# Kernel optimization log

Hardware: AMD Instinct MI355X
Metric: run time of the kernel (lower is better)

## Reference

```python
import jax, jax.numpy as jnp
import numpy as np
from jax import lax


def conv2d(x, w, b, stride, pad):
    # x: NCHW, w: OIHW (PyTorch Conv2d layout)
    y = lax.conv_general_dilated(x, w, (stride, stride), ((pad, pad), (pad, pad)),
                                 dimension_numbers=('NCHW', 'OIHW', 'NCHW'))
    return y + b[None, :, None, None]


def conv_transpose2d(x, w, b, stride, pad):
    # PyTorch ConvTranspose2d weight layout: (in_ch, out_ch, kH, kW).
    # Equivalent to a conv with lhs dilation, flipped kernel, in/out swapped.
    k = w.shape[2]
    w2 = jnp.transpose(jnp.flip(w, (2, 3)), (1, 0, 2, 3))  # (out, in, k, k)
    p = k - 1 - pad
    y = lax.conv_general_dilated(x, w2, (1, 1), ((p, p), (p, p)),
                                 lhs_dilation=(stride, stride),
                                 dimension_numbers=('NCHW', 'OIHW', 'NCHW'))
    return y + b[None, :, None, None]


def setup_inputs() -> dict:
    key = jax.random.key(0)
    ks = jax.random.split(key, 8)
    K, D = 512, 64  # num_embeddings, embedding_dim
    x = jax.random.uniform(ks[0], (32, 3, 256, 256), jnp.float32)

    def he(k, shape, fan_in):
        return jax.random.normal(k, shape, jnp.float32) * np.float32(np.sqrt(2.0 / fan_in))

    w1 = he(ks[1], (64, 3, 4, 4), 3 * 16);   b1 = jnp.zeros((64,), jnp.float32)
    w2 = he(ks[2], (D, 64, 4, 4), 64 * 16);  b2 = jnp.zeros((D,), jnp.float32)
    # codebook init: uniform(-1/K, 1/K) as in the torch module
    codebook = jax.random.uniform(ks[3], (K, D), jnp.float32, -1.0 / K, 1.0 / K)
    dw1 = he(ks[4], (D, 64, 4, 4), D * 16);  db1 = jnp.zeros((64,), jnp.float32)
    dw2 = he(ks[5], (64, 3, 4, 4), 64 * 16); db2 = jnp.zeros((3,), jnp.float32)
    return dict(x=x, w1=w1, b1=b1, w2=w2, b2=b2, codebook=codebook,
                dw1=dw1, db1=db1, dw2=dw2, db2=db2)


def reference(x, w1, b1, w2, b2, codebook, dw1, db1, dw2, db2):
    # Encoder
    z_e = jax.nn.relu(conv2d(x, w1, b1, 2, 1))
    z_e = jax.nn.relu(conv2d(z_e, w2, b2, 2, 1))  # (N, D, H/4, W/4)
    D = z_e.shape[1]
    # Faithful to torch: .view(-1, C) on contiguous NCHW (NO channel permute)
    zf = z_e.reshape(-1, D)  # (N*Hq*Wq, D) given D == Hq here numerically; rows are contiguous slices
    # ||z - e||^2 = ||z||^2 + ||e||^2 - 2 z.e  -> (M, K) distance matrix
    d = (jnp.sum(zf * zf, axis=1, keepdims=True)
         + jnp.sum(codebook * codebook, axis=1)
         - 2.0 * (zf @ codebook.T))
    idx = jnp.argmin(d, axis=1)           # (M,) int
    z_q = codebook[idx].reshape(z_e.shape)  # gather + reshape back to z_e shape
    # Decoder
    h = jax.nn.relu(conv_transpose2d(z_q, dw1, db1, 2, 1))
    x_recon = jax.nn.sigmoid(conv_transpose2d(h, dw2, db2, 2, 1))
    return x_recon, z_q
```

## Files before the change

### kernel.cpp

```cpp
#include <hip/hip_runtime.h>
#include <math.h>


typedef __attribute__((ext_vector_type(8))) short short8;
typedef __attribute__((ext_vector_type(4))) short short4v;
typedef __attribute__((ext_vector_type(4))) float f32x4;

#define MFMA16(a, b, c) __builtin_amdgcn_mfma_f32_16x16x32_bf16((a), (b), (c), 0, 0, 0)

__device__ __forceinline__ short f2bf(float f) {
  union { float f; unsigned u; } x; x.f = f;
  unsigned r = (x.u + 0x7FFFu + ((x.u >> 16) & 1u)) >> 16;
  return (short)r;
}
__device__ __forceinline__ float bf2f(short s) {
  union { unsigned u; float f; } x;
  x.u = ((unsigned)(unsigned short)s) << 16;
  return x.f;
}

__global__ __launch_bounds__(256) void k_prep(const float* __restrict__ w2,
                                              const float* __restrict__ dw1,
                                              const float* __restrict__ dw2,
                                              const float* __restrict__ cb,
                                              short* __restrict__ A2,
                                              short* __restrict__ AD1,
                                              short* __restrict__ AD2,
                                              short* __restrict__ cbb,
                                              float* __restrict__ cnm) {
  int i = blockIdx.x * 256 + threadIdx.x;
  {
    int t = i >> 12, oc = (i >> 6) & 63, c = i & 63;
    A2[i] = f2bf(w2[(oc * 64 + c) * 16 + t]);
  }
  {
    int p = i >> 14, ab = (i >> 12) & 3, oc = (i >> 6) & 63, c = i & 63;
    int kh = 1 - (p >> 1) + 2 * (ab >> 1);
    int kw = 1 - (p & 1) + 2 * (ab & 1);
    AD1[i] = f2bf(dw1[(c * 64 + oc) * 16 + kh * 4 + kw]);
  }
  if (i < 16384) {
    int p = i >> 12, ab = (i >> 10) & 3, oc = (i >> 6) & 15, c = i & 63;
    int kh = 1 - (p >> 1) + 2 * (ab >> 1);
    int kw = 1 - (p & 1) + 2 * (ab & 1);
    short v = 0;
    if (oc < 3) v = f2bf(dw2[(c * 3 + oc) * 16 + kh * 4 + kw]);
    AD2[i] = v;
  }
  if (i < 32768) cbb[i] = f2bf(cb[i]);
  if (i < 512) {
    float s = 0.f;
    for (int d = 0; d < 64; ++d) { float v = cb[i * 64 + d]; s += v * v; }
    cnm[i] = s;
  }
}

__global__ __launch_bounds__(256) void k_conv1(const float* __restrict__ x,
                                               const float* __restrict__ w1,
                                               const float* __restrict__ b1,
                                               short* __restrict__ z1T) {
  __shared__ float sW[3 * 16 * 64];
  __shared__ float sB[64];
  __shared__ float sIn[3 * 34 * 34];
  __shared__ short sOutC[256 * 72];
  const int tid = threadIdx.x;

  {
    float tw[12];
#pragma unroll
    for (int it = 0; it < 12; ++it) {
      int i = tid + 256 * it;
      int oc = i & 63, t = (i >> 6) & 15, c = i >> 10;
      tw[it] = w1[(oc * 3 + c) * 16 + t];
    }
#pragma unroll
    for (int it = 0; it < 12; ++it) sW[tid + 256 * it] = tw[it];
  }
  if (tid < 64) sB[tid] = b1[tid];

  const int b = blockIdx.x;
  const int n = b >> 6;
  const int tile = b & 63;
  const int tr = tile >> 3, tc = tile & 7;
  const int oh0 = tr * 16, ow0 = tc * 16;
  const int ih_base = oh0 * 2 - 1, iw_base = ow0 * 2 - 1;

  {
    float t[14]; bool vd[14];
#pragma unroll
    for (int it = 0; it < 14; ++it) {
      int i = tid + 256 * it;
      vd[it] = i < 3468;
      int ii = vd[it] ? i : 0;
      int c = ii / 1156;
      int rem = ii - c * 1156;
      int r = rem / 34;
      int col = rem - r * 34;
      int ih = ih_base + r, iw = iw_base + col;
      float v = 0.f;
      if (vd[it] && (unsigned)ih < 256u && (unsigned)iw < 256u)
        v = x[((n * 3 + c) * 256 + ih) * 256 + iw];
      t[it] = v;
    }
#pragma unroll
    for (int it = 0; it < 14; ++it)
      if (vd[it]) sIn[tid + 256 * it] = t[it];
  }
  __syncthreads();

  const int ty = tid >> 4, tx = tid & 15;
  float acc[64];
#pragma unroll
  for (int j = 0; j < 64; ++j) acc[j] = sB[j];

  for (int c = 0; c < 3; ++c) {
    for (int t = 0; t < 16; ++t) {
      int kh = t >> 2, kw = t & 3;
      float v = sIn[c * 1156 + (2 * ty + kh) * 34 + (2 * tx + kw)];
      const float4* wp = (const float4*)&sW[(c * 16 + t) * 64];
#pragma unroll
      for (int j = 0; j < 16; ++j) {
        float4 w4 = wp[j];
        acc[4 * j + 0] += v * w4.x;
        acc[4 * j + 1] += v * w4.y;
        acc[4 * j + 2] += v * w4.z;
        acc[4 * j + 3] += v * w4.w;
      }
    }
  }

  const int sp = ty * 16 + tx;
#pragma unroll
  for (int kk = 0; kk < 8; ++kk) {
    short8 v;
#pragma unroll
    for (int t2 = 0; t2 < 8; ++t2) {
      float r = acc[8 * kk + t2];
      v[t2] = f2bf(r > 0.f ? r : 0.f);
    }
    *(short8*)&sOutC[sp * 72 + 8 * kk] = v;
  }
  __syncthreads();
  const int r = tid >> 4, jj = tid & 15;
#pragma unroll
  for (int it = 0; it < 8; ++it) {
    int chunk = jj + 16 * it;
    int owL = chunk >> 3, c8 = chunk & 7;
    short8 v = *(const short8*)&sOutC[(r * 16 + owL) * 72 + 8 * c8];
    *(short8*)(z1T + (((long)(n * 128 + oh0 + r) * 128) + ow0 + owL) * 64 + 8 * c8) = v;
  }
}

__global__ __launch_bounds__(256) void k_conv2(const short* __restrict__ z1T,
                                               const short* __restrict__ A2,
                                               const float* __restrict__ b2,
                                               short* __restrict__ ze) {
  __shared__ char smemC[62400];
  __shared__ float sB2c[64];
  short* slab = (short*)smemC;
  short* sOut = (short*)smemC;

  const int tid = threadIdx.x;
  if (tid < 64) sB2c[tid] = b2[tid];
  const int b = blockIdx.x;
  const int n = b >> 5;
  const int oh0 = (b & 31) * 2;
  const int w = tid >> 6, l = tid & 63;
  const int row = w >> 1, mh = w & 1;
  const int e = l & 15, kg = l >> 4;
  const int ih0 = 2 * oh0 - 1;

  f32x4 acc[2][4];
#pragma unroll
  for (int mi = 0; mi < 2; ++mi)
#pragma unroll
    for (int nt = 0; nt < 4; ++nt) acc[mi][nt] = (f32x4){0.f, 0.f, 0.f, 0.f};

  for (int p = 0; p < 2; ++p) {
    const int c0 = 32 * p;
    __syncthreads();
    {
      short8 ta[7]; int off[7];
#pragma unroll
      for (int it = 0; it < 7; ++it) {
        int i = tid + 256 * it;
        int r = i / 520;
        int rem = i - r * 520;
        int iwL = rem >> 2, li = rem & 3;
        int ih = ih0 + r, iw = iwL - 1;
        off[it] = 8 * ((r * 130 + iwL) * 5 + li);
        short8 v = {0, 0, 0, 0, 0, 0, 0, 0};
        if ((unsigned)ih < 128u && (unsigned)iw < 128u)
          v = *(const short8*)(z1T + (((long)(n * 128 + ih) * 128) + iw) * 64 + c0 + 8 * li);
        ta[it] = v;
      }
#pragma unroll
      for (int it = 0; it < 7; ++it) *(short8*)&slab[off[it]] = ta[it];
    }
    {
      short8 tb[6]; int off[6]; bool vd[6];
#pragma unroll
      for (int it = 0; it < 6; ++it) {
        int i = tid + 256 * (7 + it);
        vd[it] = i < 3120;
        int ii = vd[it] ? i : 0;
        int r = ii / 520;
        int rem = ii - r * 520;
        int iwL = rem >> 2, li = rem & 3;
        int ih = ih0 + r, iw = iwL - 1;
        off[it] = 8 * ((r * 130 + iwL) * 5 + li);
        short8 v = {0, 0, 0, 0, 0, 0, 0, 0};
        if (vd[it] && (unsigned)ih < 128u && (unsigned)iw < 128u)
          v = *(const short8*)(z1T + (((long)(n * 128 + ih) * 128) + iw) * 64 + c0 + 8 * li);
        tb[it] = v;
      }
#pragma unroll
      for (int it = 0; it < 6; ++it)
        if (vd[it]) *(short8*)&slab[off[it]] = tb[it];
    }
    __syncthreads();

    for (int t = 0; t < 16; ++t) {
      const int kh = t >> 2, kw = t & 3;
      const int rL = 2 * row + kh;
      short8 aF[2], bF[4];
#pragma unroll
      for (int mi = 0; mi < 2; ++mi)
        aF[mi] = *(const short8*)(A2 + ((t * 64 + 32 * mh + 16 * mi + e) * 64) + c0 + 8 * kg);
#pragma unroll
      for (int nt = 0; nt < 4; ++nt) {
        int iwL = 2 * (nt * 16 + e) + kw;
        bF[nt] = *(const short8*)&slab[8 * ((rL * 130 + iwL) * 5 + kg)];
      }
#pragma unroll
      for (int mi = 0; mi < 2; ++mi)
#pragma unroll
        for (int nt = 0; nt < 4; ++nt)
          acc[mi][nt] = MFMA16(aF[mi], bF[nt], acc[mi][nt]);
    }
  }

  __syncthreads();
#pragma unroll
  for (int mi = 0; mi < 2; ++mi)
#pragma unroll
    for (int nt = 0; nt < 4; ++nt)
#pragma unroll
      for (int rr = 0; rr < 4; ++rr) {
        int oc = 32 * mh + 16 * mi + 4 * kg + rr;
        float v = acc[mi][nt][rr] + sB2c[oc];
        sOut[(row * 64 + oc) * 68 + nt * 16 + e] = f2bf(v > 0.f ? v : 0.f);
      }
  __syncthreads();
  {
    int oc = 32 * mh + (l >> 1);
    int half = l & 1;
#pragma unroll
    for (int j = 0; j < 8; ++j) {
      short4v v = *(const short4v*)&sOut[(row * 64 + oc) * 68 + 32 * half + 4 * j];
      *(short4v*)(ze + (((long)(n * 64 + oc) * 64) + oh0 + row) * 64 + 32 * half + 4 * j) = v;
    }
  }
}

__global__ __launch_bounds__(256) void k_vq(const short* __restrict__ zeb,
                                            const short* __restrict__ cbb,
                                            const float* __restrict__ cnm,
                                            const float* __restrict__ cb,
                                            float* __restrict__ zq,
                                            short* __restrict__ zqT) {
  const int tid = threadIdx.x;
  const int wv = tid >> 6, l = tid & 63;
  const int e = l & 15, kg = l >> 4;
  const int b = blockIdx.x;
  const int n = b >> 6, h = b & 63;

  const short* zebase = zeb + (((long)(n * 64 + 16 * wv + e) * 64) + h) * 64;
  short8 aF0 = *(const short8*)(zebase + 8 * kg);
  short8 aF1 = *(const short8*)(zebase + 32 + 8 * kg);

  float bestD[4];
  int bestI[4];
#pragma unroll
  for (int rr = 0; rr < 4; ++rr) { bestD[rr] = 3.4e38f; bestI[rr] = 0; }

  for (int ch = 0; ch < 8; ++ch) {
    f32x4 acc[4];
#pragma unroll
    for (int nt = 0; nt < 4; ++nt) {
      acc[nt] = (f32x4){0.f, 0.f, 0.f, 0.f};
      const short* cbase = cbb + (ch * 64 + nt * 16 + e) * 64;
      short8 b0 = *(const short8*)(cbase + 8 * kg);
      short8 b1 = *(const short8*)(cbase + 32 + 8 * kg);
      acc[nt] = MFMA16(aF0, b0, acc[nt]);
      acc[nt] = MFMA16(aF1, b1, acc[nt]);
    }
#pragma unroll
    for (int nt = 0; nt < 4; ++nt) {
      int code = ch * 64 + nt * 16 + e;
      float cn = cnm[code];
#pragma unroll
      for (int rr = 0; rr < 4; ++rr) {
        float d = cn - 2.f * acc[nt][rr];
        if (d < bestD[rr]) { bestD[rr] = d; bestI[rr] = code; }
      }
    }
  }
#pragma unroll
  for (int m = 1; m <= 8; m <<= 1) {
#pragma unroll
    for (int rr = 0; rr < 4; ++rr) {
      float od = __shfl_xor(bestD[rr], m);
      int oi = __shfl_xor(bestI[rr], m);
      if (od < bestD[rr] || (od == bestD[rr] && oi < bestI[rr])) {
        bestD[rr] = od; bestI[rr] = oi;
      }
    }
  }
#pragma unroll
  for (int rr = 0; rr < 4; ++rr) {
    int c = 16 * wv + 4 * kg + rr;
    int idx = bestI[rr];
    float4 v = *(const float4*)(cb + idx * 64 + 4 * e);
    *(float4*)(zq + (((long)(n * 64 + c) * 64) + h) * 64 + 4 * e) = v;
    short* qt = zqT + (((long)(n * 64 + h) * 64) + 4 * e) * 64 + c;
    qt[0] = f2bf(v.x);
    qt[64] = f2bf(v.y);
    qt[128] = f2bf(v.z);
    qt[192] = f2bf(v.w);
  }
}

__global__ __launch_bounds__(256) void k_deconv1(const short* __restrict__ zqT,
                                                 const short* __restrict__ AD1,
                                                 const float* __restrict__ db1,
                                                 short* __restrict__ hT) {
  __shared__ char smemD[34816];
  __shared__ float sBias[64];
  short* slab = (short*)smemD;
  short* sOut = (short*)smemD;

  const int tid = threadIdx.x;
  if (tid < 64) sBias[tid] = db1[tid];
  const int b = blockIdx.x;
  const int n = b >> 6, i0 = b & 63;
  const int w = tid >> 6, l = tid & 63;
  const int ph = w >> 1, pw = w & 1;
  const int e = l & 15, kg = l >> 4;

  {
    short8 t[7]; int off[7]; bool vd[7];
#pragma unroll
    for (int it = 0; it < 7; ++it) {
      int i = tid + 256 * it;
      vd[it] = i < 1584;
      int ii = vd[it] ? i : 0;
      int r = ii / 528;
      int rem = ii - r * 528;
      int iwL = rem >> 3, li = rem & 7;
      int ih = i0 - 1 + r, iw = iwL - 1;
      off[it] = (r * 66 + iwL) * 72 + 8 * li;
      short8 v = {0, 0, 0, 0, 0, 0, 0, 0};
      if (vd[it] && (unsigned)ih < 64u && (unsigned)iw < 64u)
        v = *(const short8*)(zqT + (((long)(n * 64 + ih) * 64) + iw) * 64 + 8 * li);
      t[it] = v;
    }
#pragma unroll
    for (int it = 0; it < 7; ++it)
      if (vd[it]) *(short8*)&slab[off[it]] = t[it];
  }
  __syncthreads();

  f32x4 acc[4][4];
#pragma unroll
  for (int m = 0; m < 4; ++m)
#pragma unroll
    for (int nt = 0; nt < 4; ++nt) acc[m][nt] = (f32x4){0.f, 0.f, 0.f, 0.f};

  for (int ab = 0; ab < 4; ++ab) {
    const int rL = 1 + ph - (ab >> 1);
    const int coff = pw - (ab & 1) + 1;
#pragma unroll
    for (int ks = 0; ks < 2; ++ks) {
      short8 aF[4], bF[4];
#pragma unroll
      for (int m = 0; m < 4; ++m)
        aF[m] = *(const short8*)(AD1 + (((w * 4 + ab) * 64 + 16 * m + e) * 64) + 32 * ks + 8 * kg);
#pragma unroll
      for (int nt = 0; nt < 4; ++nt) {
        int iwL = nt * 16 + e + coff;
        bF[nt] = *(const short8*)&slab[(rL * 66 + iwL) * 72 + 32 * ks + 8 * kg];
      }
#pragma unroll
      for (int m = 0; m < 4; ++m)
#pragma unroll
        for (int nt = 0; nt < 4; ++nt)
          acc[m][nt] = MFMA16(aF[m], bF[nt], acc[m][nt]);
    }
  }

  __syncthreads();
#pragma unroll
  for (int m = 0; m < 4; ++m)
#pragma unroll
    for (int nt = 0; nt < 4; ++nt) {
      int owIdx = nt * 16 + e;
      int oc0 = 16 * m + 4 * kg;
      short4v o;
#pragma unroll
      for (int rr = 0; rr < 4; ++rr) {
        float v = acc[m][nt][rr] + sBias[oc0 + rr];
        o[rr] = f2bf(v > 0.f ? v : 0.f);
      }
      *(short4v*)&sOut[((w * 64 + owIdx) * 68) + oc0] = o;
    }
  __syncthreads();
  {
    const int oh = 2 * i0 + ph;
    const int ow = 2 * l + pw;
    short* dst = hT + (((long)(n * 128 + oh) * 128) + ow) * 64;
#pragma unroll
    for (int j = 0; j < 16; ++j) {
      short4v v = *(const short4v*)&sOut[((w * 64 + l) * 68) + 4 * j];
      *(short4v*)(dst + 4 * j) = v;
    }
  }
}

__global__ __launch_bounds__(256) void k_deconv2(const short* __restrict__ hT,
                                                 const short* __restrict__ AD2,
                                                 const float* __restrict__ db2,
                                                 float* __restrict__ xr) {
  __shared__ __align__(16) char smem[38016];
  __shared__ float sB2[3];
  short* buf0 = (short*)smem;
  short* buf1 = (short*)(smem + 19008);
  float* sOut = (float*)smem;

  const int tid = threadIdx.x;
  if (tid < 3) sB2[tid] = db2[tid];
  const int b = blockIdx.x;
  const int n = b >> 7;
  const int rem0 = b & 127;
  const int q = rem0 >> 1, wh = rem0 & 1;
  const int w = tid >> 6, l = tid & 63;
  const int ph = w >> 1, pw = w & 1;
  const int e = l & 15, kg = l >> 4;

  int soff[5]; long sga[5]; bool sv[5], sin[5];
#pragma unroll
  for (int it = 0; it < 5; ++it) {
    int i = tid + 256 * it;
    sv[it] = i < 1056;
    int ii = sv[it] ? i : 0;
    int r = ii / 264;
    int rm = ii - r * 264;
    int iwL = rm >> 2, li = rm & 3;
    int ih = 2 * q - 1 + r, iw = 64 * wh - 1 + iwL;
    sin[it] = sv[it] && (unsigned)ih < 128u && (unsigned)iw < 128u;
    soff[it] = (r * 66 + iwL) * 36 + 8 * li;
    sga[it] = (((long)(n * 128 + ih) * 128) + iw) * 64 + 8 * li;
  }

  {
    short8 t0[5];
#pragma unroll
    for (int it = 0; it < 5; ++it) {
      short8 v = {0, 0, 0, 0, 0, 0, 0, 0};
      if (sin[it]) v = *(const short8*)(hT + sga[it]);
      t0[it] = v;
    }
#pragma unroll
    for (int it = 0; it < 5; ++it)
      if (sv[it]) *(short8*)&buf0[soff[it]] = t0[it];
  }
  __syncthreads();

  short8 t1[5];
#pragma unroll
  for (int it = 0; it < 5; ++it) {
    short8 v = {0, 0, 0, 0, 0, 0, 0, 0};
    if (sin[it]) v = *(const short8*)(hT + sga[it] + 32);
    t1[it] = v;
  }

  f32x4 acc[2][4];
#pragma unroll
  for (int j = 0; j < 2; ++j)
#pragma unroll
    for (int nt = 0; nt < 4; ++nt) acc[j][nt] = (f32x4){0.f, 0.f, 0.f, 0.f};

  {
    short8 aF[4];
#pragma unroll
    for (int ab = 0; ab < 4; ++ab)
      aF[ab] = *(const short8*)(AD2 + (((w * 4 + ab) * 16 + e) * 64) + 8 * kg);
#pragma unroll
    for (int ab = 0; ab < 4; ++ab) {
      const int a = ab >> 1, bb = ab & 1;
#pragma unroll
      for (int j = 0; j < 2; ++j) {
        const int rL = 1 + ph + j - a;
#pragma unroll
        for (int nt = 0; nt < 4; ++nt) {
          const int iwL = nt * 16 + e + pw - bb + 1;
          short8 bf = *(const short8*)&buf0[(rL * 66 + iwL) * 36 + 8 * kg];
          acc[j][nt] = MFMA16(aF[ab], bf, acc[j][nt]);
        }
      }
    }
  }

#pragma unroll
  for (int it = 0; it < 5; ++it)
    if (sv[it]) *(short8*)&buf1[soff[it]] = t1[it];
  __syncthreads();

  {
    short8 aF[4];
#pragma unroll
    for (int ab = 0; ab < 4; ++ab)
      aF[ab] = *(const short8*)(AD2 + (((w * 4 + ab) * 16 + e) * 64) + 32 + 8 * kg);
#pragma unroll
    for (int ab = 0; ab < 4; ++ab) {
      const int a = ab >> 1, bb = ab & 1;
#pragma unroll
      for (int j = 0; j < 2; ++j) {
        const int rL = 1 + ph + j - a;
#pragma unroll
        for (int nt = 0; nt < 4; ++nt) {
          const int iwL = nt * 16 + e + pw - bb + 1;
          short8 bf = *(const short8*)&buf1[(rL * 66 + iwL) * 36 + 8 * kg];
          acc[j][nt] = MFMA16(aF[ab], bf, acc[j][nt]);
        }
      }
    }
  }

  if (kg == 0) {
#pragma unroll
    for (int j = 0; j < 2; ++j)
#pragma unroll
      for (int nt = 0; nt < 4; ++nt) {
        int ohl = 2 * j + ph;
        int owl = 2 * (nt * 16 + e) + pw;
#pragma unroll
        for (int rr = 0; rr < 3; ++rr) {
          float v = 1.f / (1.f + expf(-(acc[j][nt][rr] + sB2[rr])));
          sOut[(rr * 4 + ohl) * 128 + owl] = v;
        }
      }
  }
  __syncthreads();
#pragma unroll
  for (int it = 0; it < 2; ++it) {
    int i = tid + 256 * it;
    if (i < 384) {
      int oc = i >> 7, r2 = i & 127;
      int ohl = r2 >> 5, c4 = r2 & 31;
      float4 v = ((const float4*)sOut)[i];
      *(float4*)(xr + (((long)(n * 3 + oc) * 256) + 4 * q + ohl) * 256 + 128 * wh + 4 * c4) = v;
    }
  }
}

extern "C" void kernel_launch(void* const* d_in, const int* in_sizes, int n_in,
                              void* d_out, int out_size, void* d_ws, size_t ws_size,
                              hipStream_t stream) {
  (void)in_sizes; (void)n_in; (void)out_size; (void)ws_size;

  const float* x   = (const float*)d_in[0];
  const float* w1  = (const float*)d_in[1];
  const float* b1  = (const float*)d_in[2];
  const float* w2  = (const float*)d_in[3];
  const float* b2  = (const float*)d_in[4];
  const float* cb  = (const float*)d_in[5];
  const float* dw1 = (const float*)d_in[6];
  const float* db1 = (const float*)d_in[7];
  const float* dw2 = (const float*)d_in[8];
  const float* db2 = (const float*)d_in[9];

  char* wsb = (char*)d_ws;
  short* z1T = (short*)wsb;
  short* zeb = (short*)(wsb + 67108864);
  short* zqT = (short*)(wsb + 83886080);
  short* A2  = (short*)(wsb + 100663296);
  short* AD1 = (short*)(wsb + 100794368);
  short* cbb = (short*)(wsb + 100925440);
  float* cnm = (float*)(wsb + 100990976);
  short* AD2 = (short*)(wsb + 100993024);
  short* hT  = z1T;

  float* xr = (float*)d_out;
  float* zq = (float*)d_out + 6291456;

  k_prep<<<256, 256, 0, stream>>>(w2, dw1, dw2, cb, A2, AD1, AD2, cbb, cnm);
  k_conv1<<<2048, 256, 0, stream>>>(x, w1, b1, z1T);
  k_conv2<<<1024, 256, 0, stream>>>(z1T, A2, b2, zeb);
  k_vq<<<2048, 256, 0, stream>>>(zeb, cbb, cnm, cb, zq, zqT);
  k_deconv1<<<2048, 256, 0, stream>>>(zqT, AD1, db1, hT);
  k_deconv2<<<4096, 256, 0, stream>>>(hT, AD2, db2, xr);
}
```

Measured before the change: 458.2 us.

## Enlarge deconv2 tiles to full-width 8-row bands and stage VQ transpose in LDS

k_vq now writes the bf16 transposed codebook vectors into a shared-memory tile and then stores them as coalesced 16-byte rows, replacing scattered 2-byte global stores. k_deconv2 moves from 4096 blocks of 256 threads, each covering 4 output rows by half the width, to 1024 blocks of 512 threads, each covering 8 full-width output rows. Each block loads one input slab and reuses it across more outputs, which lowers halo reloads and block count. The single slab is reused for both channel halves with an extra barrier. This drops the previous double-buffer overlap, and the larger LDS footprint may lower occupancy.

Result: slower. 471.6 us (+2.9%).

```diff
diff --git a/kernel.cpp b/kernel.cpp
--- a/kernel.cpp
+++ b/kernel.cpp
@@ -269,6 +269,7 @@
                                             const float* __restrict__ cb,
                                             float* __restrict__ zq,
                                             short* __restrict__ zqT) {
+  __shared__ short sT[64 * 68];
   const int tid = threadIdx.x;
   const int wv = tid >> 6, l = tid & 63;
   const int e = l & 15, kg = l >> 4;
@@ -323,11 +324,19 @@
     int idx = bestI[rr];
     float4 v = *(const float4*)(cb + idx * 64 + 4 * e);
     *(float4*)(zq + (((long)(n * 64 + c) * 64) + h) * 64 + 4 * e) = v;
-    short* qt = zqT + (((long)(n * 64 + h) * 64) + 4 * e) * 64 + c;
-    qt[0] = f2bf(v.x);
-    qt[64] = f2bf(v.y);
-    qt[128] = f2bf(v.z);
-    qt[192] = f2bf(v.w);
+    sT[(4 * e + 0) * 68 + c] = f2bf(v.x);
+    sT[(4 * e + 1) * 68 + c] = f2bf(v.y);
+    sT[(4 * e + 2) * 68 + c] = f2bf(v.z);
+    sT[(4 * e + 3) * 68 + c] = f2bf(v.w);
+  }
+  __syncthreads();
+  {
+    int wq = tid >> 2, hq = tid & 3;
+    short8 v0 = *(const short8*)&sT[wq * 68 + 16 * hq];
+    short8 v1 = *(const short8*)&sT[wq * 68 + 16 * hq + 8];
+    short* dst = zqT + (((long)(n * 64 + h) * 64) + wq) * 64 + 16 * hq;
+    *(short8*)dst = v0;
+    *(short8*)(dst + 8) = v1;
   }
 }
 
@@ -427,140 +436,139 @@
   }
 }
 
-__global__ __launch_bounds__(256) void k_deconv2(const short* __restrict__ hT,
+__global__ __launch_bounds__(512) void k_deconv2(const short* __restrict__ hT,
                                                  const short* __restrict__ AD2,
                                                  const float* __restrict__ db2,
                                                  float* __restrict__ xr) {
-  __shared__ __align__(16) char smem[38016];
+  __shared__ __align__(16) char smem[56160];
   __shared__ float sB2[3];
-  short* buf0 = (short*)smem;
-  short* buf1 = (short*)(smem + 19008);
+  short* slab = (short*)smem;
   float* sOut = (float*)smem;
 
   const int tid = threadIdx.x;
   if (tid < 3) sB2[tid] = db2[tid];
   const int b = blockIdx.x;
-  const int n = b >> 7;
-  const int rem0 = b & 127;
-  const int q = rem0 >> 1, wh = rem0 & 1;
+  const int n = b >> 5;
+  const int band = b & 31;
   const int w = tid >> 6, l = tid & 63;
-  const int ph = w >> 1, pw = w & 1;
+  const int ph = w >> 2, pw = (w >> 1) & 1, chf = w & 1;
+  const int p = ph * 2 + pw;
   const int e = l & 15, kg = l >> 4;
 
-  int soff[5]; long sga[5]; bool sv[5], sin[5];
-#pragma unroll
-  for (int it = 0; it < 5; ++it) {
-    int i = tid + 256 * it;
-    sv[it] = i < 1056;
+  int soff[7]; long sga[7]; bool sv[7], sinb[7];
+#pragma unroll
+  for (int it = 0; it < 7; ++it) {
+    int i = tid + 512 * it;
+    sv[it] = i < 3120;
     int ii = sv[it] ? i : 0;
-    int r = ii / 264;
-    int rm = ii - r * 264;
+    int r = ii / 520;
+    int rm = ii - r * 520;
     int iwL = rm >> 2, li = rm & 3;
-    int ih = 2 * q - 1 + r, iw = 64 * wh - 1 + iwL;
-    sin[it] = sv[it] && (unsigned)ih < 128u && (unsigned)iw < 128u;
-    soff[it] = (r * 66 + iwL) * 36 + 8 * li;
+    int ih = 4 * band - 1 + r, iw = iwL - 1;
+    sinb[it] = sv[it] && (unsigned)ih < 128u && (unsigned)iw < 128u;
+    soff[it] = (r * 130 + iwL) * 36 + 8 * li;
     sga[it] = (((long)(n * 128 + ih) * 128) + iw) * 64 + 8 * li;
   }
 
   {
-    short8 t0[5];
-#pragma unroll
-    for (int it = 0; it < 5; ++it) {
+    short8 t0[7];
+#pragma unroll
+    for (int it = 0; it < 7; ++it) {
       short8 v = {0, 0, 0, 0, 0, 0, 0, 0};
-      if (sin[it]) v = *(const short8*)(hT + sga[it]);
+      if (sinb[it]) v = *(const short8*)(hT + sga[it]);
       t0[it] = v;
     }
 #pragma unroll
-    for (int it = 0; it < 5; ++it)
-      if (sv[it]) *(short8*)&buf0[soff[it]] = t0[it];
-  }
-  __syncthreads();
-
-  short8 t1[5];
-#pragma unroll
-  for (int it = 0; it < 5; ++it) {
+    for (int it = 0; it < 7; ++it)
+      if (sv[it]) *(short8*)&slab[soff[it]] = t0[it];
+  }
+  __syncthreads();
+
+  short8 t1[7];
+#pragma unroll
+  for (int it = 0; it < 7; ++it) {
     short8 v = {0, 0, 0, 0, 0, 0, 0, 0};
-    if (sin[it]) v = *(const short8*)(hT + sga[it] + 32);
+    if (sinb[it]) v = *(const short8*)(hT + sga[it] + 32);
     t1[it] = v;
   }
 
-  f32x4 acc[2][4];
-#pragma unroll
-  for (int j = 0; j < 2; ++j)
+  f32x4 acc[4][4];
+#pragma unroll
+  for (int j = 0; j < 4; ++j)
 #pragma unroll
     for (int nt = 0; nt < 4; ++nt) acc[j][nt] = (f32x4){0.f, 0.f, 0.f, 0.f};
 
+  const int colBase = 64 * chf + e + pw + 1;
   {
     short8 aF[4];
 #pragma unroll
     for (int ab = 0; ab < 4; ++ab)
-      aF[ab] = *(const short8*)(AD2 + (((w * 4 + ab) * 16 + e) * 64) + 8 * kg);
+      aF[ab] = *(const short8*)(AD2 + (((p * 4 + ab) * 16 + e) * 64) + 8 * kg);
 #pragma unroll
     for (int ab = 0; ab < 4; ++ab) {
       const int a = ab >> 1, bb = ab & 1;
 #pragma unroll
-      for (int j = 0; j < 2; ++j) {
-        const int rL = 1 + ph + j - a;
+      for (int j = 0; j < 4; ++j) {
+        const int rL = j + ph - a + 1;
 #pragma unroll
         for (int nt = 0; nt < 4; ++nt) {
-          const int iwL = nt * 16 + e + pw - bb + 1;
-          short8 bf = *(const short8*)&buf0[(rL * 66 + iwL) * 36 + 8 * kg];
+          const int iwL = nt * 16 + colBase - bb;
+          short8 bf = *(const short8*)&slab[(rL * 130 + iwL) * 36 + 8 * kg];
           acc[j][nt] = MFMA16(aF[ab], bf, acc[j][nt]);
         }
       }
     }
   }
-
-#pragma unroll
-  for (int it = 0; it < 5; ++it)
-    if (sv[it]) *(short8*)&buf1[soff[it]] = t1[it];
-  __syncthreads();
-
+  __syncthreads();
+
+#pragma unroll
+  for (int it = 0; it < 7; ++it)
+    if (sv[it]) *(short8*)&slab[soff[it]] = t1[it];
+  __syncthreads();
   {
     short8 aF[4];
 #pragma unroll
     for (int ab = 0; ab < 4; ++ab)
-      aF[ab] = *(const short8*)(AD2 + (((w * 4 + ab) * 16 + e) * 64) + 32 + 8 * kg);
+      aF[ab] = *(const short8*)(AD2 + (((p * 4 + ab) * 16 + e) * 64) + 32 + 8 * kg);
 #pragma unroll
     for (int ab = 0; ab < 4; ++ab) {
       const int a = ab >> 1, bb = ab & 1;
 #pragma unroll
-      for (int j = 0; j < 2; ++j) {
-        const int rL = 1 + ph + j - a;
+      for (int j = 0; j < 4; ++j) {
+        const int rL = j + ph - a + 1;
 #pragma unroll
         for (int nt = 0; nt < 4; ++nt) {
-          const int iwL = nt * 16 + e + pw - bb + 1;
-          short8 bf = *(const short8*)&buf1[(rL * 66 + iwL) * 36 + 8 * kg];
+          const int iwL = nt * 16 + colBase - bb;
+          short8 bf = *(const short8*)&slab[(rL * 130 + iwL) * 36 + 8 * kg];
           acc[j][nt] = MFMA16(aF[ab], bf, acc[j][nt]);
         }
       }
     }
   }
+  __syncthreads();
 
   if (kg == 0) {
 #pragma unroll
-    for (int j = 0; j < 2; ++j)
+    for (int j = 0; j < 4; ++j)
 #pragma unroll
       for (int nt = 0; nt < 4; ++nt) {
         int ohl = 2 * j + ph;
-        int owl = 2 * (nt * 16 + e) + pw;
+        int ow = 2 * (64 * chf + nt * 16 + e) + pw;
 #pragma unroll
         for (int rr = 0; rr < 3; ++rr) {
           float v = 1.f / (1.f + expf(-(acc[j][nt][rr] + sB2[rr])));
-          sOut[(rr * 4 + ohl) * 128 + owl] = v;
+          sOut[(rr * 8 + ohl) * 256 + ow] = v;
         }
       }
   }
   __syncthreads();
 #pragma unroll
-  for (int it = 0; it < 2; ++it) {
-    int i = tid + 256 * it;
-    if (i < 384) {
-      int oc = i >> 7, r2 = i & 127;
-      int ohl = r2 >> 5, c4 = r2 & 31;
-      float4 v = ((const float4*)sOut)[i];
-      *(float4*)(xr + (((long)(n * 3 + oc) * 256) + 4 * q + ohl) * 256 + 128 * wh + 4 * c4) = v;
-    }
+  for (int it = 0; it < 3; ++it) {
+    int i = tid + 512 * it;
+    int oc = i / 512, rem = i - oc * 512;
+    int ohl = rem >> 6, c4 = rem & 63;
+    float4 v = ((const float4*)sOut)[i];
+    *(float4*)(xr + (((long)(n * 3 + oc) * 256) + 8 * band + ohl) * 256 + 4 * c4) = v;
   }
 }
 
@@ -599,5 +607,5 @@
   k_conv2<<<1024, 256, 0, stream>>>(z1T, A2, b2, zeb);
   k_vq<<<2048, 256, 0, stream>>>(zeb, cbb, cnm, cb, zq, zqT);
   k_deconv1<<<2048, 256, 0, stream>>>(zqT, AD1, db1, hT);
-  k_deconv2<<<4096, 256, 0, stream>>>(hT, AD2, db2, xr);
-}
+  k_deconv2<<<1024, 512, 0, stream>>>(hT, AD2, db2, xr);
+}
```
